# Kernel optimization log

Measured on AMD Instinct MI355X. Metric: run time of the kernel, lower is better.

Reference implementation:

```python
import jax, jax.numpy as jnp
import numpy as np

ATT_TIMES = 2
EPS = 1e-12  # torch F.normalize eps

N_NODES = 200000
EMB_DIM = 256
ATT_NUM = 2


def setup_inputs() -> dict:
    key = jax.random.key(0)
    k1, k2 = jax.random.split(key)
    x = jax.random.normal(k1, (N_NODES, EMB_DIM), dtype=jnp.float32)
    # glorot/xavier-normal init for the att_num projection matrices W_i
    std = float(np.sqrt(2.0 / (EMB_DIM + EMB_DIM)))
    W = jax.random.normal(k2, (ATT_NUM, EMB_DIM, EMB_DIM), dtype=jnp.float32) * std
    return {"x": x, "W": W}


def _one_attention(x, Wi):
    """One attention head (att_style='dot', att_weight=True), iterated ATT_TIMES."""
    xi = x
    out = None
    for _ in range(ATT_TIMES):
        temp = jnp.mean(xi, axis=0, keepdims=True)          # (1, D)
        h_avg = jnp.tanh(temp @ Wi)                          # (1, D)
        # 'dot' style: interact with W = identity -> scores = x @ h_avg^T, (N, 1)
        scores = xi @ h_avg.T                                # (N, 1)
        # F.normalize(p=1, dim=1) on an (N,1) column: divide by max(|v|, eps)
        norm = jnp.maximum(jnp.sum(jnp.abs(scores), axis=1, keepdims=True), EPS)
        att = jax.nn.sigmoid(scores / norm)                  # (N, 1)
        out = att.T @ xi                                     # (1, D)
        xi = xi * att                                        # re-weight for next round
    return out


def reference(x, W):
    att_num = W.shape[0]
    outs = [_one_attention(x, W[i]) for i in range(att_num)]
    return jnp.concatenate(outs, axis=1)                     # (1, att_num * D)
```

## Files before the change

### kernel.cpp

```cpp
#include <hip/hip_runtime.h>
#include <math.h>

#define NROWS 200000
#define D 256
#define F4 64

#define NBLK 500
#define CHUNK 400
#define ITERS 25

#define WS_H1 0
#define WS_H2 512
#define WS_A  1024
#define WS_P1 401024
#define WS_P2 529024

__device__ __forceinline__ float att_sigmoid(float s) {
    float t = s / fmaxf(fabsf(s), 1e-12f);
    return 1.0f / (1.0f + __expf(-t));
}

__device__ __forceinline__ float wave_sum(float v) {
#pragma unroll
    for (int off = 1; off < 64; off <<= 1) v += __shfl_xor(v, off);
    return v;
}

__device__ __forceinline__ float dot4(float4 a, float4 b) {
    return fmaf(a.x, b.x, fmaf(a.y, b.y, fmaf(a.z, b.z, a.w * b.w)));
}

__global__ void __launch_bounds__(256) colsum_kernel(const float* __restrict__ x,
                                                     float* __restrict__ part) {
    const int tid = threadIdx.x, lane = tid & 63, wv = tid >> 6;
    const float4* x4 = reinterpret_cast<const float4*>(x);
    const size_t base = (size_t)(blockIdx.x * CHUNK + wv * 4) * F4 + lane;
    float4 cur[4], nxt[4];
#pragma unroll
    for (int j = 0; j < 4; ++j) cur[j] = x4[base + j * F4];
    float4 accA = make_float4(0.f, 0.f, 0.f, 0.f);
    float4 accB = make_float4(0.f, 0.f, 0.f, 0.f);
    for (int it = 0; it < ITERS; ++it) {
        if (it + 1 < ITERS) {
            size_t nb = base + (size_t)(it + 1) * 16 * F4;
#pragma unroll
            for (int j = 0; j < 4; ++j) nxt[j] = x4[nb + j * F4];
        }
        accA.x += cur[0].x + cur[1].x; accB.x += cur[2].x + cur[3].x;
        accA.y += cur[0].y + cur[1].y; accB.y += cur[2].y + cur[3].y;
        accA.z += cur[0].z + cur[1].z; accB.z += cur[2].z + cur[3].z;
        accA.w += cur[0].w + cur[1].w; accB.w += cur[2].w + cur[3].w;
        if (it + 1 < ITERS) {
#pragma unroll
            for (int j = 0; j < 4; ++j) cur[j] = nxt[j];
        }
    }
    accA.x += accB.x; accA.y += accB.y; accA.z += accB.z; accA.w += accB.w;
    __shared__ float4 sh[256];
    sh[tid] = accA;
    __syncthreads();
    if (tid < 64) {
        float4 a = sh[tid], b = sh[tid + 64], c = sh[tid + 128], d = sh[tid + 192];
        float4 s;
        s.x = (a.x + b.x) + (c.x + d.x);
        s.y = (a.y + b.y) + (c.y + d.y);
        s.z = (a.z + b.z) + (c.z + d.z);
        s.w = (a.w + b.w) + (c.w + d.w);
        reinterpret_cast<float4*>(part + blockIdx.x * 256)[tid] = s;
    }
}

__global__ void __launch_bounds__(256) hproj_fused(const float* __restrict__ W,
                                                   const float* __restrict__ part,
                                                   int width, int headColMul, float scale,
                                                   float* __restrict__ hout) {
    const int head = blockIdx.x;
    const int tid = threadIdx.x, lane = tid & 63, wv = tid >> 6;
    const float* p = part + head * headColMul + lane * 4;
    float4 s = make_float4(0.f, 0.f, 0.f, 0.f);
    for (int i = 0; i < 25; ++i) {
        float4 v[5];
#pragma unroll
        for (int k = 0; k < 5; ++k)
            v[k] = *reinterpret_cast<const float4*>(p + (size_t)(wv + (i * 5 + k) * 4) * width);
#pragma unroll
        for (int k = 0; k < 5; ++k) {
            s.x += v[k].x; s.y += v[k].y; s.z += v[k].z; s.w += v[k].w;
        }
    }
    __shared__ float4 red[4][64];
    __shared__ float vbuf[D];
    red[wv][lane] = s;
    __syncthreads();
    if (tid < 64) {
        float4 a = red[0][tid], b = red[1][tid], c = red[2][tid], d = red[3][tid];
        vbuf[tid * 4 + 0] = ((a.x + b.x) + (c.x + d.x)) * scale;
        vbuf[tid * 4 + 1] = ((a.y + b.y) + (c.y + d.y)) * scale;
        vbuf[tid * 4 + 2] = ((a.z + b.z) + (c.z + d.z)) * scale;
        vbuf[tid * 4 + 3] = ((a.w + b.w) + (c.w + d.w)) * scale;
    }
    __syncthreads();
    const float* Wh = W + head * D * D;
    float acc = 0.0f;
#pragma unroll 8
    for (int k = 0; k < D; ++k) acc = fmaf(vbuf[k], Wh[k * D + tid], acc);
    hout[head * D + tid] = tanhf(acc);
}

__global__ void __launch_bounds__(256) pass1_kernel(const float* __restrict__ x,
                                                    float* __restrict__ ws) {
    const float* h = ws + WS_H1;
    float* aA0 = ws + WS_A;
    float* aA1 = ws + WS_A + NROWS;
    float* part = ws + WS_P2;
    const int tid = threadIdx.x, lane = tid & 63, wv = tid >> 6;
    const int r0 = blockIdx.x * CHUNK + wv * 4;
    const float4* x4 = reinterpret_cast<const float4*>(x);
    const float4 h0v = reinterpret_cast<const float4*>(h)[lane];
    const float4 h1v = reinterpret_cast<const float4*>(h + D)[lane];
    float4 acc0 = make_float4(0.f, 0.f, 0.f, 0.f);
    float4 acc1 = make_float4(0.f, 0.f, 0.f, 0.f);
    const size_t base = (size_t)r0 * F4 + lane;
    float4 cur[4], nxt[4];
#pragma unroll
    for (int j = 0; j < 4; ++j) cur[j] = x4[base + j * F4];
    for (int it = 0; it < ITERS; ++it) {
        if (it + 1 < ITERS) {
            size_t nb = base + (size_t)(it + 1) * 16 * F4;
#pragma unroll
            for (int j = 0; j < 4; ++j) nxt[j] = x4[nb + j * F4];
        }
        float d0[4], d1[4];
#pragma unroll
        for (int j = 0; j < 4; ++j) { d0[j] = dot4(cur[j], h0v); d1[j] = dot4(cur[j], h1v); }
#pragma unroll
        for (int j = 0; j < 4; ++j) { d0[j] = wave_sum(d0[j]); d1[j] = wave_sum(d1[j]); }
        float a0[4], a1[4];
#pragma unroll
        for (int j = 0; j < 4; ++j) {
            a0[j] = att_sigmoid(d0[j]);
            a1[j] = att_sigmoid(d1[j]);
            acc0.x = fmaf(a0[j], cur[j].x, acc0.x);
            acc0.y = fmaf(a0[j], cur[j].y, acc0.y);
            acc0.z = fmaf(a0[j], cur[j].z, acc0.z);
            acc0.w = fmaf(a0[j], cur[j].w, acc0.w);
            acc1.x = fmaf(a1[j], cur[j].x, acc1.x);
            acc1.y = fmaf(a1[j], cur[j].y, acc1.y);
            acc1.z = fmaf(a1[j], cur[j].z, acc1.z);
            acc1.w = fmaf(a1[j], cur[j].w, acc1.w);
        }
        const int rb = r0 + it * 16;
        if (lane == 0)
            *reinterpret_cast<float4*>(aA0 + rb) = make_float4(a0[0], a0[1], a0[2], a0[3]);
        else if (lane == 1)
            *reinterpret_cast<float4*>(aA1 + rb) = make_float4(a1[0], a1[1], a1[2], a1[3]);
        if (it + 1 < ITERS) {
#pragma unroll
            for (int j = 0; j < 4; ++j) cur[j] = nxt[j];
        }
    }
    __shared__ float4 sh[2][256];
    sh[0][tid] = acc0;
    sh[1][tid] = acc1;
    __syncthreads();
    if (tid < 128) {
        int hh = tid >> 6;
        int t = tid & 63;
        float4 a = sh[hh][t], b = sh[hh][t + 64], c = sh[hh][t + 128], d = sh[hh][t + 192];
        float4 s;
        s.x = (a.x + b.x) + (c.x + d.x);
        s.y = (a.y + b.y) + (c.y + d.y);
        s.z = (a.z + b.z) + (c.z + d.z);
        s.w = (a.w + b.w) + (c.w + d.w);
        reinterpret_cast<float4*>(part + blockIdx.x * 512)[tid] = s;
    }
}

__global__ void __launch_bounds__(256) pass2_kernel(const float* __restrict__ x,
                                                    float* __restrict__ ws) {
    const float* h = ws + WS_H2;
    const float* aA0 = ws + WS_A;
    const float* aA1 = ws + WS_A + NROWS;
    float* part = ws + WS_P2;
    const int tid = threadIdx.x, lane = tid & 63, wv = tid >> 6;
    const int r0 = blockIdx.x * CHUNK + wv * 4;
    const float4* x4 = reinterpret_cast<const float4*>(x);
    const float4 h0v = reinterpret_cast<const float4*>(h)[lane];
    const float4 h1v = reinterpret_cast<const float4*>(h + D)[lane];
    float4 acc0 = make_float4(0.f, 0.f, 0.f, 0.f);
    float4 acc1 = make_float4(0.f, 0.f, 0.f, 0.f);
    const size_t base = (size_t)r0 * F4 + lane;
    float4 cur[4], nxt[4];
    float4 caa0, caa1, naa0, naa1;
#pragma unroll
    for (int j = 0; j < 4; ++j) cur[j] = x4[base + j * F4];
    caa0 = *reinterpret_cast<const float4*>(aA0 + r0);
    caa1 = *reinterpret_cast<const float4*>(aA1 + r0);
    for (int it = 0; it < ITERS; ++it) {
        if (it + 1 < ITERS) {
            size_t nb = base + (size_t)(it + 1) * 16 * F4;
#pragma unroll
            for (int j = 0; j < 4; ++j) nxt[j] = x4[nb + j * F4];
            naa0 = *reinterpret_cast<const float4*>(aA0 + r0 + (it + 1) * 16);
            naa1 = *reinterpret_cast<const float4*>(aA1 + r0 + (it + 1) * 16);
        }
        float d0[4], d1[4];
#pragma unroll
        for (int j = 0; j < 4; ++j) { d0[j] = dot4(cur[j], h0v); d1[j] = dot4(cur[j], h1v); }
#pragma unroll
        for (int j = 0; j < 4; ++j) { d0[j] = wave_sum(d0[j]); d1[j] = wave_sum(d1[j]); }
        float w0[4], w1[4];
        w0[0] = att_sigmoid(caa0.x * d0[0]) * caa0.x;
        w0[1] = att_sigmoid(caa0.y * d0[1]) * caa0.y;
        w0[2] = att_sigmoid(caa0.z * d0[2]) * caa0.z;
        w0[3] = att_sigmoid(caa0.w * d0[3]) * caa0.w;
        w1[0] = att_sigmoid(caa1.x * d1[0]) * caa1.x;
        w1[1] = att_sigmoid(caa1.y * d1[1]) * caa1.y;
        w1[2] = att_sigmoid(caa1.z * d1[2]) * caa1.z;
        w1[3] = att_sigmoid(caa1.w * d1[3]) * caa1.w;
#pragma unroll
        for (int j = 0; j < 4; ++j) {
            acc0.x = fmaf(w0[j], cur[j].x, acc0.x);
            acc0.y = fmaf(w0[j], cur[j].y, acc0.y);
            acc0.z = fmaf(w0[j], cur[j].z, acc0.z);
            acc0.w = fmaf(w0[j], cur[j].w, acc0.w);
            acc1.x = fmaf(w1[j], cur[j].x, acc1.x);
            acc1.y = fmaf(w1[j], cur[j].y, acc1.y);
            acc1.z = fmaf(w1[j], cur[j].z, acc1.z);
            acc1.w = fmaf(w1[j], cur[j].w, acc1.w);
        }
        if (it + 1 < ITERS) {
#pragma unroll
            for (int j = 0; j < 4; ++j) cur[j] = nxt[j];
            caa0 = naa0; caa1 = naa1;
        }
    }
    __shared__ float4 sh[2][256];
    sh[0][tid] = acc0;
    sh[1][tid] = acc1;
    __syncthreads();
    if (tid < 128) {
        int hh = tid >> 6;
        int t = tid & 63;
        float4 a = sh[hh][t], b = sh[hh][t + 64], c = sh[hh][t + 128], d = sh[hh][t + 192];
        float4 s;
        s.x = (a.x + b.x) + (c.x + d.x);
        s.y = (a.y + b.y) + (c.y + d.y);
        s.z = (a.z + b.z) + (c.z + d.z);
        s.w = (a.w + b.w) + (c.w + d.w);
        reinterpret_cast<float4*>(part + blockIdx.x * 512)[tid] = s;
    }
}

__global__ void __launch_bounds__(256) out_reduce(const float* __restrict__ part,
                                                  float* __restrict__ out) {
    const int head = blockIdx.x;
    const int tid = threadIdx.x, lane = tid & 63, wv = tid >> 6;
    const float* p = part + head * 256 + lane * 4;
    float4 s = make_float4(0.f, 0.f, 0.f, 0.f);
    for (int i = 0; i < 25; ++i) {
        float4 v[5];
#pragma unroll
        for (int k = 0; k < 5; ++k)
            v[k] = *reinterpret_cast<const float4*>(p + (size_t)(wv + (i * 5 + k) * 4) * 512);
#pragma unroll
        for (int k = 0; k < 5; ++k) {
            s.x += v[k].x; s.y += v[k].y; s.z += v[k].z; s.w += v[k].w;
        }
    }
    __shared__ float4 red[4][64];
    red[wv][lane] = s;
    __syncthreads();
    if (tid < 64) {
        float4 a = red[0][tid], b = red[1][tid], c = red[2][tid], d = red[3][tid];
        float4 o;
        o.x = (a.x + b.x) + (c.x + d.x);
        o.y = (a.y + b.y) + (c.y + d.y);
        o.z = (a.z + b.z) + (c.z + d.z);
        o.w = (a.w + b.w) + (c.w + d.w);
        reinterpret_cast<float4*>(out + head * 256)[tid] = o;
    }
}

extern "C" void kernel_launch(void* const* d_in, const int* in_sizes, int n_in,
                              void* d_out, int out_size, void* d_ws, size_t ws_size,
                              hipStream_t stream) {
    const float* x = (const float*)d_in[0];
    const float* W = (const float*)d_in[1];
    float* out = (float*)d_out;
    float* ws = (float*)d_ws;

    colsum_kernel<<<dim3(NBLK), dim3(256), 0, stream>>>(x, ws + WS_P1);
    hproj_fused<<<dim3(2), dim3(256), 0, stream>>>(W, ws + WS_P1, 256, 0, 1.0f / NROWS, ws + WS_H1);
    pass1_kernel<<<dim3(NBLK), dim3(256), 0, stream>>>(x, ws);
    hproj_fused<<<dim3(2), dim3(256), 0, stream>>>(W, ws + WS_P2, 512, 256, 1.0f / NROWS, ws + WS_H2);
    pass2_kernel<<<dim3(NBLK), dim3(256), 0, stream>>>(x, ws);
    out_reduce<<<dim3(2), dim3(256), 0, stream>>>(ws + WS_P2, out);
}
```

Measured before the change: 167.2 us.

## Cache a bf16 copy of x during colsum and run both attention passes on it

The column-sum pass now also writes a bf16 (round-to-nearest-even) copy of x into the workspace. Both attention passes read that compact copy instead of fp32 x, using a 32-lane-per-row layout with 8 elements per lane. This cuts HBM traffic for the later passes at the cost of an extra write and reduced input precision. The fp32 path is kept as a fallback when the workspace is too small.

```diff
diff --git a/kernel.cpp b/kernel.cpp
--- a/kernel.cpp
+++ b/kernel.cpp
@@ -14,6 +14,7 @@
 #define WS_A  1024
 #define WS_P1 401024
 #define WS_P2 529024
+#define WS_XB 785024
 
 __device__ __forceinline__ float att_sigmoid(float s) {
     float t = s / fmaxf(fabsf(s), 1e-12f);
@@ -30,11 +31,35 @@
     return fmaf(a.x, b.x, fmaf(a.y, b.y, fmaf(a.z, b.z, a.w * b.w)));
 }
 
-__global__ void __launch_bounds__(256) colsum_kernel(const float* __restrict__ x,
-                                                     float* __restrict__ part) {
+__device__ __forceinline__ void acc4(float4& acc, float s, const float4& v) {
+    acc.x = fmaf(s, v.x, acc.x);
+    acc.y = fmaf(s, v.y, acc.y);
+    acc.z = fmaf(s, v.z, acc.z);
+    acc.w = fmaf(s, v.w, acc.w);
+}
+
+__device__ __forceinline__ unsigned int packbf2(float a, float b) {
+    unsigned int ua = __float_as_uint(a);
+    unsigned int ub = __float_as_uint(b);
+    ua = (ua + 0x7FFFu + ((ua >> 16) & 1u)) >> 16;
+    ub = (ub + 0x7FFFu + ((ub >> 16) & 1u)) >> 16;
+    return ua | (ub << 16);
+}
+
+__device__ __forceinline__ void unpack8(uint4 q, float* f) {
+    f[0] = __uint_as_float(q.x << 16); f[1] = __uint_as_float(q.x & 0xFFFF0000u);
+    f[2] = __uint_as_float(q.y << 16); f[3] = __uint_as_float(q.y & 0xFFFF0000u);
+    f[4] = __uint_as_float(q.z << 16); f[5] = __uint_as_float(q.z & 0xFFFF0000u);
+    f[6] = __uint_as_float(q.w << 16); f[7] = __uint_as_float(q.w & 0xFFFF0000u);
+}
+
+__global__ void __launch_bounds__(256) colsum_cast_kernel(const float* __restrict__ x,
+                                                          float* __restrict__ part,
+                                                          uint2* __restrict__ xb2) {
     const int tid = threadIdx.x, lane = tid & 63, wv = tid >> 6;
     const float4* x4 = reinterpret_cast<const float4*>(x);
-    const size_t base = (size_t)(blockIdx.x * CHUNK + wv * 4) * F4 + lane;
+    const int r0 = blockIdx.x * CHUNK + wv * 4;
+    const size_t base = (size_t)r0 * F4 + lane;
     float4 cur[4], nxt[4];
 #pragma unroll
     for (int j = 0; j < 4; ++j) cur[j] = x4[base + j * F4];
@@ -50,6 +75,12 @@
         accA.y += cur[0].y + cur[1].y; accB.y += cur[2].y + cur[3].y;
         accA.z += cur[0].z + cur[1].z; accB.z += cur[2].z + cur[3].z;
         accA.w += cur[0].w + cur[1].w; accB.w += cur[2].w + cur[3].w;
+        const int rb = r0 + it * 16;
+#pragma unroll
+        for (int j = 0; j < 4; ++j) {
+            xb2[(size_t)(rb + j) * 64 + lane] =
+                make_uint2(packbf2(cur[j].x, cur[j].y), packbf2(cur[j].z, cur[j].w));
+        }
         if (it + 1 < ITERS) {
 #pragma unroll
             for (int j = 0; j < 4; ++j) cur[j] = nxt[j];
@@ -66,27 +97,22 @@
         s.y = (a.y + b.y) + (c.y + d.y);
         s.z = (a.z + b.z) + (c.z + d.z);
         s.w = (a.w + b.w) + (c.w + d.w);
-        reinterpret_cast<float4*>(part + blockIdx.x * 256)[tid] = s;
+        reinterpret_cast<float4*>(part)[blockIdx.x * 64 + tid] = s;
     }
 }
 
 __global__ void __launch_bounds__(256) hproj_fused(const float* __restrict__ W,
                                                    const float* __restrict__ part,
-                                                   int width, int headColMul, float scale,
+                                                   int width4, int headOff4, float scale,
                                                    float* __restrict__ hout) {
     const int head = blockIdx.x;
     const int tid = threadIdx.x, lane = tid & 63, wv = tid >> 6;
-    const float* p = part + head * headColMul + lane * 4;
+    const float4* p4 = reinterpret_cast<const float4*>(part) + head * headOff4 + lane;
     float4 s = make_float4(0.f, 0.f, 0.f, 0.f);
-    for (int i = 0; i < 25; ++i) {
-        float4 v[5];
-#pragma unroll
-        for (int k = 0; k < 5; ++k)
-            v[k] = *reinterpret_cast<const float4*>(p + (size_t)(wv + (i * 5 + k) * 4) * width);
-#pragma unroll
-        for (int k = 0; k < 5; ++k) {
-            s.x += v[k].x; s.y += v[k].y; s.z += v[k].z; s.w += v[k].w;
-        }
+#pragma unroll 5
+    for (int r = wv; r < NBLK; r += 4) {
+        float4 v = p4[(size_t)r * width4];
+        s.x += v.x; s.y += v.y; s.z += v.z; s.w += v.w;
     }
     __shared__ float4 red[4][64];
     __shared__ float vbuf[D];
@@ -105,6 +131,180 @@
 #pragma unroll 8
     for (int k = 0; k < D; ++k) acc = fmaf(vbuf[k], Wh[k * D + tid], acc);
     hout[head * D + tid] = tanhf(acc);
+}
+
+__global__ void __launch_bounds__(256) pass1_bf16_kernel(const uint4* __restrict__ xb,
+                                                         float* __restrict__ ws) {
+    const float* h = ws + WS_H1;
+    float* aA0 = ws + WS_A;
+    float* aA1 = ws + WS_A + NROWS;
+    float* part = ws + WS_P2;
+    const int tid = threadIdx.x, lane = tid & 63, wv = tid >> 6;
+    const int hi = lane >> 5, chunk = lane & 31, c0 = chunk * 8;
+    const int r0 = blockIdx.x * CHUNK + wv * 4;
+    float hh0[8], hh1[8];
+#pragma unroll
+    for (int k = 0; k < 8; ++k) { hh0[k] = h[c0 + k]; hh1[k] = h[D + c0 + k]; }
+    float acc0[8], acc1[8];
+#pragma unroll
+    for (int k = 0; k < 8; ++k) { acc0[k] = 0.f; acc1[k] = 0.f; }
+    const size_t base = (size_t)r0 * 32;
+    uint4 cur0 = xb[base + lane];
+    uint4 cur1 = xb[base + 64 + lane];
+    for (int it = 0; it < ITERS; ++it) {
+        uint4 nxt0, nxt1;
+        if (it + 1 < ITERS) {
+            const size_t nb = base + (size_t)(it + 1) * 512;
+            nxt0 = xb[nb + lane];
+            nxt1 = xb[nb + 64 + lane];
+        }
+        float f0[8], f1[8];
+        unpack8(cur0, f0);
+        unpack8(cur1, f1);
+        float d00 = 0.f, d01 = 0.f, d10 = 0.f, d11 = 0.f;
+#pragma unroll
+        for (int k = 0; k < 8; ++k) {
+            d00 = fmaf(f0[k], hh0[k], d00); d10 = fmaf(f0[k], hh1[k], d10);
+            d01 = fmaf(f1[k], hh0[k], d01); d11 = fmaf(f1[k], hh1[k], d11);
+        }
+#pragma unroll
+        for (int off = 1; off < 32; off <<= 1) {
+            d00 += __shfl_xor(d00, off); d01 += __shfl_xor(d01, off);
+            d10 += __shfl_xor(d10, off); d11 += __shfl_xor(d11, off);
+        }
+        float a00 = att_sigmoid(d00), a01 = att_sigmoid(d01);
+        float a10 = att_sigmoid(d10), a11 = att_sigmoid(d11);
+        const int rb = r0 + it * 16;
+        if (chunk == 0) {
+            aA0[rb + hi] = a00; aA0[rb + 2 + hi] = a01;
+            aA1[rb + hi] = a10; aA1[rb + 2 + hi] = a11;
+        }
+#pragma unroll
+        for (int k = 0; k < 8; ++k) {
+            acc0[k] = fmaf(a00, f0[k], acc0[k]); acc0[k] = fmaf(a01, f1[k], acc0[k]);
+            acc1[k] = fmaf(a10, f0[k], acc1[k]); acc1[k] = fmaf(a11, f1[k], acc1[k]);
+        }
+        cur0 = nxt0; cur1 = nxt1;
+    }
+    __shared__ float lds[256][17];
+#pragma unroll
+    for (int k = 0; k < 8; ++k) { lds[tid][k] = acc0[k]; lds[tid][8 + k] = acc1[k]; }
+    __syncthreads();
+    float s0 = 0.f, s1 = 0.f;
+#pragma unroll
+    for (int g = 0; g < 8; ++g) {
+        s0 += lds[g * 32 + (tid >> 3)][tid & 7];
+        s1 += lds[g * 32 + (tid >> 3)][8 + (tid & 7)];
+    }
+    part[blockIdx.x * 512 + tid] = s0;
+    part[blockIdx.x * 512 + 256 + tid] = s1;
+}
+
+__global__ void __launch_bounds__(256) pass2_bf16_kernel(const uint4* __restrict__ xb,
+                                                         float* __restrict__ ws) {
+    const float* h = ws + WS_H2;
+    const float* aA0 = ws + WS_A;
+    const float* aA1 = ws + WS_A + NROWS;
+    float* part = ws + WS_P2;
+    const int tid = threadIdx.x, lane = tid & 63, wv = tid >> 6;
+    const int hi = lane >> 5, chunk = lane & 31, c0 = chunk * 8;
+    const int r0 = blockIdx.x * CHUNK + wv * 4;
+    float hh0[8], hh1[8];
+#pragma unroll
+    for (int k = 0; k < 8; ++k) { hh0[k] = h[c0 + k]; hh1[k] = h[D + c0 + k]; }
+    float acc0[8], acc1[8];
+#pragma unroll
+    for (int k = 0; k < 8; ++k) { acc0[k] = 0.f; acc1[k] = 0.f; }
+    const size_t base = (size_t)r0 * 32;
+    uint4 cur0 = xb[base + lane];
+    uint4 cur1 = xb[base + 64 + lane];
+    for (int it = 0; it < ITERS; ++it) {
+        uint4 nxt0, nxt1;
+        if (it + 1 < ITERS) {
+            const size_t nb = base + (size_t)(it + 1) * 512;
+            nxt0 = xb[nb + lane];
+            nxt1 = xb[nb + 64 + lane];
+        }
+        const int rb = r0 + it * 16;
+        float aa00 = aA0[rb + hi], aa01 = aA0[rb + 2 + hi];
+        float aa10 = aA1[rb + hi], aa11 = aA1[rb + 2 + hi];
+        float f0[8], f1[8];
+        unpack8(cur0, f0);
+        unpack8(cur1, f1);
+        float d00 = 0.f, d01 = 0.f, d10 = 0.f, d11 = 0.f;
+#pragma unroll
+        for (int k = 0; k < 8; ++k) {
+            d00 = fmaf(f0[k], hh0[k], d00); d10 = fmaf(f0[k], hh1[k], d10);
+            d01 = fmaf(f1[k], hh0[k], d01); d11 = fmaf(f1[k], hh1[k], d11);
+        }
+#pragma unroll
+        for (int off = 1; off < 32; off <<= 1) {
+            d00 += __shfl_xor(d00, off); d01 += __shfl_xor(d01, off);
+            d10 += __shfl_xor(d10, off); d11 += __shfl_xor(d11, off);
+        }
+        float w00 = att_sigmoid(aa00 * d00) * aa00;
+        float w01 = att_sigmoid(aa01 * d01) * aa01;
+        float w10 = att_sigmoid(aa10 * d10) * aa10;
+        float w11 = att_sigmoid(aa11 * d11) * aa11;
+#pragma unroll
+        for (int k = 0; k < 8; ++k) {
+            acc0[k] = fmaf(w00, f0[k], acc0[k]); acc0[k] = fmaf(w01, f1[k], acc0[k]);
+            acc1[k] = fmaf(w10, f0[k], acc1[k]); acc1[k] = fmaf(w11, f1[k], acc1[k]);
+        }
+        cur0 = nxt0; cur1 = nxt1;
+    }
+    __shared__ float lds[256][17];
+#pragma unroll
+    for (int k = 0; k < 8; ++k) { lds[tid][k] = acc0[k]; lds[tid][8 + k] = acc1[k]; }
+    __syncthreads();
+    float s0 = 0.f, s1 = 0.f;
+#pragma unroll
+    for (int g = 0; g < 8; ++g) {
+        s0 += lds[g * 32 + (tid >> 3)][tid & 7];
+        s1 += lds[g * 32 + (tid >> 3)][8 + (tid & 7)];
+    }
+    part[blockIdx.x * 512 + tid] = s0;
+    part[blockIdx.x * 512 + 256 + tid] = s1;
+}
+
+__global__ void __launch_bounds__(256) colsum_kernel(const float* __restrict__ x,
+                                                     float* __restrict__ part) {
+    const int tid = threadIdx.x, lane = tid & 63, wv = tid >> 6;
+    const float4* x4 = reinterpret_cast<const float4*>(x);
+    const size_t base = (size_t)(blockIdx.x * CHUNK + wv * 4) * F4 + lane;
+    float4 cur[4], nxt[4];
+#pragma unroll
+    for (int j = 0; j < 4; ++j) cur[j] = x4[base + j * F4];
+    float4 accA = make_float4(0.f, 0.f, 0.f, 0.f);
+    float4 accB = make_float4(0.f, 0.f, 0.f, 0.f);
+    for (int it = 0; it < ITERS; ++it) {
+        if (it + 1 < ITERS) {
+            size_t nb = base + (size_t)(it + 1) * 16 * F4;
+#pragma unroll
+            for (int j = 0; j < 4; ++j) nxt[j] = x4[nb + j * F4];
+        }
+        accA.x += cur[0].x + cur[1].x; accB.x += cur[2].x + cur[3].x;
+        accA.y += cur[0].y + cur[1].y; accB.y += cur[2].y + cur[3].y;
+        accA.z += cur[0].z + cur[1].z; accB.z += cur[2].z + cur[3].z;
+        accA.w += cur[0].w + cur[1].w; accB.w += cur[2].w + cur[3].w;
+        if (it + 1 < ITERS) {
+#pragma unroll
+            for (int j = 0; j < 4; ++j) cur[j] = nxt[j];
+        }
+    }
+    accA.x += accB.x; accA.y += accB.y; accA.z += accB.z; accA.w += accB.w;
+    __shared__ float4 sh[256];
+    sh[tid] = accA;
+    __syncthreads();
+    if (tid < 64) {
+        float4 a = sh[tid], b = sh[tid + 64], c = sh[tid + 128], d = sh[tid + 192];
+        float4 s;
+        s.x = (a.x + b.x) + (c.x + d.x);
+        s.y = (a.y + b.y) + (c.y + d.y);
+        s.z = (a.z + b.z) + (c.z + d.z);
+        s.w = (a.w + b.w) + (c.w + d.w);
+        reinterpret_cast<float4*>(part)[blockIdx.x * 64 + tid] = s;
+    }
 }
 
 __global__ void __launch_bounds__(256) pass1_kernel(const float* __restrict__ x,
@@ -140,14 +340,8 @@
         for (int j = 0; j < 4; ++j) {
             a0[j] = att_sigmoid(d0[j]);
             a1[j] = att_sigmoid(d1[j]);
-            acc0.x = fmaf(a0[j], cur[j].x, acc0.x);
-            acc0.y = fmaf(a0[j], cur[j].y, acc0.y);
-            acc0.z = fmaf(a0[j], cur[j].z, acc0.z);
-            acc0.w = fmaf(a0[j], cur[j].w, acc0.w);
-            acc1.x = fmaf(a1[j], cur[j].x, acc1.x);
-            acc1.y = fmaf(a1[j], cur[j].y, acc1.y);
-            acc1.z = fmaf(a1[j], cur[j].z, acc1.z);
-            acc1.w = fmaf(a1[j], cur[j].w, acc1.w);
+            acc4(acc0, a0[j], cur[j]);
+            acc4(acc1, a1[j], cur[j]);
         }
         const int rb = r0 + it * 16;
         if (lane == 0)
@@ -172,7 +366,7 @@
         s.y = (a.y + b.y) + (c.y + d.y);
         s.z = (a.z + b.z) + (c.z + d.z);
         s.w = (a.w + b.w) + (c.w + d.w);
-        reinterpret_cast<float4*>(part + blockIdx.x * 512)[tid] = s;
+        reinterpret_cast<float4*>(part)[blockIdx.x * 128 + tid] = s;
     }
 }
 
@@ -220,14 +414,8 @@
         w1[3] = att_sigmoid(caa1.w * d1[3]) * caa1.w;
 #pragma unroll
         for (int j = 0; j < 4; ++j) {
-            acc0.x = fmaf(w0[j], cur[j].x, acc0.x);
-            acc0.y = fmaf(w0[j], cur[j].y, acc0.y);
-            acc0.z = fmaf(w0[j], cur[j].z, acc0.z);
-            acc0.w = fmaf(w0[j], cur[j].w, acc0.w);
-            acc1.x = fmaf(w1[j], cur[j].x, acc1.x);
-            acc1.y = fmaf(w1[j], cur[j].y, acc1.y);
-            acc1.z = fmaf(w1[j], cur[j].z, acc1.z);
-            acc1.w = fmaf(w1[j], cur[j].w, acc1.w);
+            acc4(acc0, w0[j], cur[j]);
+            acc4(acc1, w1[j], cur[j]);
         }
         if (it + 1 < ITERS) {
 #pragma unroll
@@ -248,7 +436,7 @@
         s.y = (a.y + b.y) + (c.y + d.y);
         s.z = (a.z + b.z) + (c.z + d.z);
         s.w = (a.w + b.w) + (c.w + d.w);
-        reinterpret_cast<float4*>(part + blockIdx.x * 512)[tid] = s;
+        reinterpret_cast<float4*>(part)[blockIdx.x * 128 + tid] = s;
     }
 }
 
@@ -256,17 +444,12 @@
                                                   float* __restrict__ out) {
     const int head = blockIdx.x;
     const int tid = threadIdx.x, lane = tid & 63, wv = tid >> 6;
-    const float* p = part + head * 256 + lane * 4;
+    const float4* p4 = reinterpret_cast<const float4*>(part) + head * 64 + lane;
     float4 s = make_float4(0.f, 0.f, 0.f, 0.f);
-    for (int i = 0; i < 25; ++i) {
-        float4 v[5];
-#pragma unroll
-        for (int k = 0; k < 5; ++k)
-            v[k] = *reinterpret_cast<const float4*>(p + (size_t)(wv + (i * 5 + k) * 4) * 512);
-#pragma unroll
-        for (int k = 0; k < 5; ++k) {
-            s.x += v[k].x; s.y += v[k].y; s.z += v[k].z; s.w += v[k].w;
-        }
+#pragma unroll 5
+    for (int r = wv; r < NBLK; r += 4) {
+        float4 v = p4[(size_t)r * 128];
+        s.x += v.x; s.y += v.y; s.z += v.z; s.w += v.w;
     }
     __shared__ float4 red[4][64];
     red[wv][lane] = s;
@@ -278,7 +461,7 @@
         o.y = (a.y + b.y) + (c.y + d.y);
         o.z = (a.z + b.z) + (c.z + d.z);
         o.w = (a.w + b.w) + (c.w + d.w);
-        reinterpret_cast<float4*>(out + head * 256)[tid] = o;
+        reinterpret_cast<float4*>(out)[head * 64 + tid] = o;
     }
 }
 
@@ -290,10 +473,22 @@
     float* out = (float*)d_out;
     float* ws = (float*)d_ws;
 
-    colsum_kernel<<<dim3(NBLK), dim3(256), 0, stream>>>(x, ws + WS_P1);
-    hproj_fused<<<dim3(2), dim3(256), 0, stream>>>(W, ws + WS_P1, 256, 0, 1.0f / NROWS, ws + WS_H1);
-    pass1_kernel<<<dim3(NBLK), dim3(256), 0, stream>>>(x, ws);
-    hproj_fused<<<dim3(2), dim3(256), 0, stream>>>(W, ws + WS_P2, 512, 256, 1.0f / NROWS, ws + WS_H2);
-    pass2_kernel<<<dim3(NBLK), dim3(256), 0, stream>>>(x, ws);
-    out_reduce<<<dim3(2), dim3(256), 0, stream>>>(ws + WS_P2, out);
-}
+    const size_t need = (size_t)WS_XB * 4 + (size_t)NROWS * 512;
+    if (ws_size >= need) {
+        uint2* xb2 = reinterpret_cast<uint2*>(ws + WS_XB);
+        const uint4* xb4 = reinterpret_cast<const uint4*>(ws + WS_XB);
+        colsum_cast_kernel<<<dim3(NBLK), dim3(256), 0, stream>>>(x, ws + WS_P1, xb2);
+        hproj_fused<<<dim3(2), dim3(256), 0, stream>>>(W, ws + WS_P1, 64, 0, 1.0f / NROWS, ws + WS_H1);
+        pass1_bf16_kernel<<<dim3(NBLK), dim3(256), 0, stream>>>(xb4, ws);
+        hproj_fused<<<dim3(2), dim3(256), 0, stream>>>(W, ws + WS_P2, 128, 64, 1.0f / NROWS, ws + WS_H2);
+        pass2_bf16_kernel<<<dim3(NBLK), dim3(256), 0, stream>>>(xb4, ws);
+        out_reduce<<<dim3(2), dim3(256), 0, stream>>>(ws + WS_P2, out);
+    } else {
+        colsum_kernel<<<dim3(NBLK), dim3(256), 0, stream>>>(x, ws + WS_P1);
+        hproj_fused<<<dim3(2), dim3(256), 0, stream>>>(W, ws + WS_P1, 64, 0, 1.0f / NROWS, ws + WS_H1);
+        pass1_kernel<<<dim3(NBLK), dim3(256), 0, stream>>>(x, ws);
+        hproj_fused<<<dim3(2), dim3(256), 0, stream>>>(W, ws + WS_P2, 128, 64, 1.0f / NROWS, ws + WS_H2);
+        pass2_kernel<<<dim3(NBLK), dim3(256), 0, stream>>>(x, ws);
+        out_reduce<<<dim3(2), dim3(256), 0, stream>>>(ws + WS_P2, out);
+    }
+}
```

After: 157.5 us. 5.8% less time.
